# Performance work log

Measured on AMD Instinct MI355X. Metric: run time of the kernel, lower is better.

The kernel has to match this reference:

```python
import jax, jax.numpy as jnp
import numpy as np
from jax import lax

N_SKILLS = 10000
EMB = 128
HEADS = 4
DH = EMB // HEADS  # 32 per-head out channels
E_EDGES = 320000
B, T = 256, 200
RNN_H = 256
NEG_SLOPE = 0.2  # GATv2 LeakyReLU default


def setup_inputs() -> dict:
    key = jax.random.key(0)
    ks = jax.random.split(key, 32)
    inp = {}
    inp["skills_in"] = jax.random.randint(ks[0], (B, T), 0, N_SKILLS)
    inp["resp_in"] = jax.random.randint(ks[1], (B, T), 0, 2)
    lengths = jnp.sort(jax.random.randint(ks[2], (B,), 5, T + 1))[::-1]
    inp["lengths"] = lengths.at[0].set(T)  # enforce_sorted=True, max len = T
    inp["edge_index"] = jax.random.randint(ks[3], (2, E_EDGES), 0, N_SKILLS)
    inp["edge_weight"] = jax.random.uniform(ks[4], (E_EDGES,), dtype=jnp.float32)
    sc = 0.05
    inp["skill_emb_w"] = jax.random.normal(ks[5], (N_SKILLS, EMB), jnp.float32) * sc
    kidx = 6
    for l in range(2):
        inp[f"g{l}_Wl"] = jax.random.normal(ks[kidx + 0], (EMB, EMB), jnp.float32) * sc
        inp[f"g{l}_bl"] = jnp.zeros((EMB,), jnp.float32)
        inp[f"g{l}_Wr"] = jax.random.normal(ks[kidx + 1], (EMB, EMB), jnp.float32) * sc
        inp[f"g{l}_br"] = jnp.zeros((EMB,), jnp.float32)
        inp[f"g{l}_We"] = jax.random.normal(ks[kidx + 2], (EMB, 1), jnp.float32) * sc
        inp[f"g{l}_att"] = jax.random.normal(ks[kidx + 3], (HEADS, DH), jnp.float32) * sc
        inp[f"g{l}_bias"] = jnp.zeros((EMB,), jnp.float32)
        kidx += 4
    inp["resp_emb_w"] = jax.random.normal(ks[14], (2, EMB), jnp.float32) * sc
    inp["gru_Wih"] = jax.random.normal(ks[15], (3 * RNN_H, EMB), jnp.float32) * sc
    inp["gru_Whh"] = jax.random.normal(ks[16], (3 * RNN_H, RNN_H), jnp.float32) * sc
    inp["gru_bih"] = jnp.zeros((3 * RNN_H,), jnp.float32)
    inp["gru_bhh"] = jnp.zeros((3 * RNN_H,), jnp.float32)
    inp["proj_W"] = jax.random.normal(ks[17], (EMB, RNN_H), jnp.float32) * sc
    inp["proj_b"] = jnp.zeros((EMB,), jnp.float32)
    return inp


def _add_self_loops(edge_index, edge_weight):
    # PyG add_remaining_self_loops with fill_value='mean': loop attr = mean of
    # incoming edge attrs per target node (0 if no incoming edges).
    src, dst = edge_index[0], edge_index[1]
    ea = edge_weight.reshape(-1, 1)
    s = jax.ops.segment_sum(ea, dst, num_segments=N_SKILLS)
    c = jax.ops.segment_sum(jnp.ones_like(ea), dst, num_segments=N_SKILLS)
    loop_attr = s / jnp.maximum(c, 1.0)
    ar = jnp.arange(N_SKILLS, dtype=src.dtype)
    return (jnp.concatenate([src, ar]), jnp.concatenate([dst, ar]),
            jnp.concatenate([ea, loop_attr], axis=0))


def _gatv2_layer(h, src, dst, ea, Wl, bl, Wr, br, We, att, bias):
    xl = (h @ Wl.T + bl).reshape(-1, HEADS, DH)   # [N,H,D] lin_l
    xr = (h @ Wr.T + br).reshape(-1, HEADS, DH)   # [N,H,D] lin_r
    ee = (ea @ We.T).reshape(-1, HEADS, DH)       # [E,H,D] lin_edge (no bias)
    m = xl[src] + xr[dst] + ee                    # per-edge message pre-act
    m_act = jnp.where(m > 0, m, NEG_SLOPE * m)
    e = jnp.einsum('ehd,hd->eh', m_act, att)      # attention logits
    emax = jax.ops.segment_max(e, dst, num_segments=N_SKILLS)
    a = jnp.exp(e - emax[dst])
    denom = jax.ops.segment_sum(a, dst, num_segments=N_SKILLS)
    alpha = a / (denom[dst] + 1e-16)              # softmax over incoming edges
    out = jax.ops.segment_sum(alpha[:, :, None] * xl[src], dst,
                              num_segments=N_SKILLS)
    return out.reshape(-1, HEADS * DH) + bias


def _gru(x, lengths, Wih, Whh, bih, bhh):
    # Packed GRU emulation: state frozen and output zeroed past each length.
    Bb, Tt, _ = x.shape
    H = Whh.shape[1]
    xg = jnp.einsum('bte,ge->btg', x, Wih) + bih  # [B,T,3H], gates r|z|n
    mask = (jnp.arange(Tt)[None, :] < lengths[:, None])  # [B,T]

    def step(h, inp):
        xg_t, m_t = inp  # [B,3H], [B,1]
        hg = h @ Whh.T + bhh
        xr, xz, xn = jnp.split(xg_t, 3, axis=-1)
        hr, hz, hn = jnp.split(hg, 3, axis=-1)
        r = jax.nn.sigmoid(xr + hr)
        z = jax.nn.sigmoid(xz + hz)
        n = jnp.tanh(xn + r * hn)
        h_new = (1.0 - z) * n + z * h
        h_keep = jnp.where(m_t, h_new, h)
        y = jnp.where(m_t, h_new, 0.0)  # pad_packed_sequence zero-pads
        return h_keep, y

    h0 = jnp.zeros((Bb, H), x.dtype)
    _, ys = lax.scan(step, h0, (xg.transpose(1, 0, 2), mask.T[:, :, None]))
    return ys.transpose(1, 0, 2)  # [B,T,H]


def reference(skills_in, resp_in, lengths, edge_index, edge_weight,
              skill_emb_w,
              g0_Wl, g0_bl, g0_Wr, g0_br, g0_We, g0_att, g0_bias,
              g1_Wl, g1_bl, g1_Wr, g1_br, g1_We, g1_att, g1_bias,
              resp_emb_w, gru_Wih, gru_Whh, gru_bih, gru_bhh,
              proj_W, proj_b):
    src, dst, ea = _add_self_loops(edge_index, edge_weight)
    h = skill_emb_w
    h = jax.nn.elu(_gatv2_layer(h, src, dst, ea, g0_Wl, g0_bl, g0_Wr, g0_br,
                                g0_We, g0_att, g0_bias))
    h = jax.nn.elu(_gatv2_layer(h, src, dst, ea, g1_Wl, g1_bl, g1_Wr, g1_br,
                                g1_We, g1_att, g1_bias))
    skill_embs = h  # [N,EMB] (dropout is identity in eval)
    x = skill_embs[skills_in] + resp_emb_w[resp_in]  # [B,T,EMB]
    hseq = _gru(x, lengths, gru_Wih, gru_Whh, gru_bih, gru_bhh)
    h_proj = hseq @ proj_W.T + proj_b  # [B,T,EMB]
    return (h_proj, skill_embs)
```

## Files before the change

### kernel.cpp

```cpp
#include <hip/hip_runtime.h>

#define N_NODES 10000
#define EMB     128
#define NE      320000
#define NE_TOT  330000
#define NB      256
#define NTT     200
#define RH      256
#define G3      768

typedef unsigned short u16;
typedef u16    u16x8  __attribute__((ext_vector_type(8)));
typedef __bf16 bf16x8 __attribute__((ext_vector_type(8)));
typedef float  f32x4  __attribute__((ext_vector_type(4)));

static __device__ __forceinline__ float bf2f(u16 u){
  unsigned int x = ((unsigned int)u) << 16;
  return __builtin_bit_cast(float, x);
}
static __device__ __forceinline__ u16 f2bf(float f){
  unsigned int x = __builtin_bit_cast(unsigned int, f);
  x += 0x7fffu + ((x >> 16) & 1u);
  return (u16)(x >> 16);
}

static __device__ __forceinline__ void stage16(const u16* g, u16* lds_wavebase, u16* lds_lane){
#if __has_builtin(__builtin_amdgcn_global_load_lds)
  __builtin_amdgcn_global_load_lds(
      (const __attribute__((address_space(1))) unsigned int*)g,
      (__attribute__((address_space(3))) unsigned int*)lds_wavebase, 16, 0, 0);
  (void)lds_lane;
#else
  *(u16x8*)lds_lane = *(const u16x8*)g;
#endif
}

static __device__ __forceinline__ float self4(f32x4 v, int r){
  float lo = (r&1) ? v[1] : v[0];
  float hi = (r&1) ? v[3] : v[2];
  return (r&2) ? hi : lo;
}
static __device__ __forceinline__ f32x4 seltile(f32x4 a, f32x4 b, f32x4 c, f32x4 d, int jt){
  f32x4 r;
  #pragma unroll
  for(int e=0;e<4;++e){
    float ab = (jt&1) ? b[e] : a[e];
    float cd = (jt&1) ? d[e] : c[e];
    r[e] = (jt&2) ? cd : ab;
  }
  return r;
}

__global__ void k_deg(const int* __restrict__ eidx, const float* __restrict__ ew,
                      int* __restrict__ deg, float* __restrict__ wsum){
  int i = blockIdx.x*256 + threadIdx.x;
  if(i >= NE) return;
  int d = eidx[NE + i];
  atomicAdd(&deg[d], 1);
  atomicAdd(&wsum[d], ew[i]);
}

__global__ __launch_bounds__(1024) void k_scan(const int* __restrict__ deg,
                      float* __restrict__ wsum, int* __restrict__ off){
  __shared__ int part[1024];
  int tid = threadIdx.x;
  int n0 = tid*10;
  int s = 0;
  for(int i=0;i<10;++i){ int n=n0+i; if(n<N_NODES) s += deg[n]+1; }
  part[tid] = s;
  for(int i=0;i<10;++i){
    int n=n0+i;
    if(n<N_NODES){ int d=deg[n]; wsum[n] = wsum[n] / (float)(d>1?d:1); }
  }
  __syncthreads();
  for(int st=1; st<1024; st<<=1){
    int v = (tid>=st) ? part[tid-st] : 0;
    __syncthreads();
    part[tid] += v;
    __syncthreads();
  }
  int base = tid ? part[tid-1] : 0;
  for(int i=0;i<10;++i){ int n=n0+i; if(n<N_NODES){ off[n]=base; base += deg[n]+1; } }
  if(tid==999) off[N_NODES] = base;
}

__global__ void k_scatter(const int* __restrict__ eidx, const float* __restrict__ ew,
                          const float* __restrict__ la, const int* __restrict__ off,
                          int* __restrict__ fill, int* __restrict__ csrs, float* __restrict__ csrw){
  int i = blockIdx.x*256 + threadIdx.x;
  if(i >= NE_TOT) return;
  int s, d; float w;
  if(i < NE){ s = eidx[i]; d = eidx[NE+i]; w = ew[i]; }
  else      { int n = i-NE; s=n; d=n; w = la[n]; }
  int pos = off[d] + atomicAdd(&fill[d], 1);
  csrs[pos] = s; csrw[pos] = w;
}

#define WB_W   393216
#define WB_TOT (WB_W + N_NODES*EMB)
__global__ __launch_bounds__(256) void k_cvtall(
    const float* __restrict__ g0l, const float* __restrict__ g0r,
    const float* __restrict__ g1l, const float* __restrict__ g1r,
    const float* __restrict__ wih, const float* __restrict__ whh,
    const float* __restrict__ pw, const float* __restrict__ emb,
    u16* __restrict__ wb){
  int i = blockIdx.x*256 + threadIdx.x;
  if(i >= WB_TOT) return;
  float v;
  if(i < 65536){
    int seg = i >> 14, r = i & 16383;
    const float* s = (seg==0) ? g0l : (seg==1) ? g0r : (seg==2) ? g1l : g1r;
    v = s[r];
  } else if(i < 163840){ v = wih[i - 65536]; }
  else if(i < 360448){ v = whh[i - 163840]; }
  else if(i < WB_W)  { v = pw [i - 360448]; }
  else               { v = emb[i - WB_W]; }
  wb[i] = f2bf(v);
}

__global__ __launch_bounds__(256) void k_gather(
    const float* __restrict__ embN, const float* __restrict__ remb,
    const int* __restrict__ skills, const int* __restrict__ resp,
    u16* __restrict__ xemb){
  int i = blockIdx.x*256 + threadIdx.x;
  if(i >= NB*NTT*EMB/8) return;
  int row = i >> 4;
  int g8  = (i & 15) * 8;
  const float* ar = embN + (size_t)skills[row]*EMB + g8;
  const float* rr = remb + (size_t)resp[row]*EMB + g8;
  u16x8 v;
  #pragma unroll
  for(int e=0;e<8;++e) v[e] = f2bf(ar[e] + rr[e]);
  *(u16x8*)(xemb + (size_t)row*EMB + g8) = v;
}

template<int AMODE, bool OUTF32, int MI>
__global__ __launch_bounds__(256) void k_gemm(
    const u16* __restrict__ Av, const u16* __restrict__ W, const float* __restrict__ bias,
    void* __restrict__ out,
    int M, int N, int K,
    int t0, int chk,
    const int* __restrict__ lens)
{
  int tid = threadIdx.x;
  int wid = tid >> 6, l = tid & 63;
  int lr = l & 15, lg = l >> 4;
  int bm = blockIdx.x*(MI*64) + wid*(MI*16);
  int bn = blockIdx.y*64;
  f32x4 acc[MI][4] = {};
  int nk = K >> 5;
  for(int kt=0; kt<nk; ++kt){
    int k0 = kt*32 + lg*8;
    bf16x8 af[MI];
    #pragma unroll
    for(int mi=0; mi<MI; ++mi){
      int row = bm + mi*16 + lr;
      u16x8 v = {0,0,0,0,0,0,0,0};
      if(row < M){
        if constexpr(AMODE == 3){
          int b = row / chk, tt = row - b*chk;
          int arow = b*NTT + t0 + tt;
          v = *(const u16x8*)(Av + (size_t)arow*K + k0);
        } else {
          v = *(const u16x8*)(Av + (size_t)row*K + k0);
        }
      }
      af[mi] = __builtin_bit_cast(bf16x8, v);
    }
    #pragma unroll
    for(int nt=0; nt<4; ++nt){
      int col = bn + nt*16 + lr;
      u16x8 wv = *(const u16x8*)(W + (size_t)col*K + k0);
      bf16x8 bfr = __builtin_bit_cast(bf16x8, wv);
      #pragma unroll
      for(int mi=0; mi<MI; ++mi)
        acc[mi][nt] = __builtin_amdgcn_mfma_f32_16x16x32_bf16(af[mi], bfr, acc[mi][nt], 0,0,0);
    }
  }
  #pragma unroll
  for(int mi=0; mi<MI; ++mi){
    #pragma unroll
    for(int nt=0; nt<4; ++nt){
      int col = bn + nt*16 + lr;
      float bc = bias[col];
      #pragma unroll
      for(int r=0; r<4; ++r){
        int row = bm + mi*16 + lg*4 + r;
        if(row >= M) continue;
        float v = acc[mi][nt][r] + bc;
        if(lens){ int b = row/NTT; int t = row - b*NTT; if(t >= lens[b]) v = bc; }
        if constexpr(OUTF32) ((float*)out)[(size_t)row*N + col] = v;
        else                 ((u16*) out)[(size_t)row*N + col] = f2bf(v);
      }
    }
  }
}

template<bool BF16OUT>
__global__ __launch_bounds__(256) void k_attn(
    const int* __restrict__ off, const int* __restrict__ csrs, const float* __restrict__ csrw,
    const u16* __restrict__ xl, const u16* __restrict__ xr,
    const float* __restrict__ We, const float* __restrict__ att, const float* __restrict__ bias,
    float* __restrict__ houtF, u16* __restrict__ houtB)
{
  int wid = threadIdx.x >> 6, l = threadIdx.x & 63;
  int n = blockIdx.x*4 + wid;
  int d0 = 2*l;
  const unsigned int* xl2 = (const unsigned int*)xl;
  unsigned int xru = ((const unsigned int*)xr)[n*64 + l];
  float xrx = bf2f((u16)xru), xry = bf2f((u16)(xru>>16));
  float wex = We[d0],  wey = We[d0+1];
  float atx = att[d0], aty = att[d0+1];
  int p0 = off[n], p1 = off[n+1];
  float mx = -1e30f;
  for(int p=p0; p<p1; ++p){
    int s = csrs[p]; float w = csrw[p];
    unsigned int u = xl2[s*64 + l];
    float ax = bf2f((u16)u)       + xrx + w*wex;
    float ay = bf2f((u16)(u>>16)) + xry + w*wey;
    ax = ax > 0.f ? ax : 0.2f*ax;
    ay = ay > 0.f ? ay : 0.2f*ay;
    float c = ax*atx + ay*aty;
    c += __shfl_xor(c,1); c += __shfl_xor(c,2); c += __shfl_xor(c,4); c += __shfl_xor(c,8);
    mx = fmaxf(mx, c);
  }
  float den = 0.f, a0 = 0.f, a1 = 0.f;
  for(int p=p0; p<p1; ++p){
    int s = csrs[p]; float w = csrw[p];
    unsigned int u = xl2[s*64 + l];
    float xlx = bf2f((u16)u), xly = bf2f((u16)(u>>16));
    float ax = xlx + xrx + w*wex;
    float ay = xly + xry + w*wey;
    ax = ax > 0.f ? ax : 0.2f*ax;
    ay = ay > 0.f ? ay : 0.2f*ay;
    float c = ax*atx + ay*aty;
    c += __shfl_xor(c,1); c += __shfl_xor(c,2); c += __shfl_xor(c,4); c += __shfl_xor(c,8);
    float al = __expf(c - mx);
    den += al; a0 += al*xlx; a1 += al*xly;
  }
  float inv = 1.f/(den + 1e-16f);
  float o0 = a0*inv + bias[d0];
  float o1 = a1*inv + bias[d0+1];
  o0 = o0 > 0.f ? o0 : (__expf(o0) - 1.f);
  o1 = o1 > 0.f ? o1 : (__expf(o1) - 1.f);
  if constexpr(BF16OUT){
    houtB[n*EMB + d0]   = f2bf(o0);
    houtB[n*EMB + d0+1] = f2bf(o1);
  } else {
    houtF[n*EMB + d0]   = o0;
    houtF[n*EMB + d0+1] = o1;
  }
}


#define DECLW(nt) f32x4 wf_##nt##_0, wf_##nt##_1, wf_##nt##_2, wf_##nt##_3, \
                        wf_##nt##_4, wf_##nt##_5, wf_##nt##_6, wf_##nt##_7;

#define LDW1(nt,kt) { u16x8 wv = *(const u16x8*)(wr + (kt)*32 + lg*8); \
  wf_##nt##_##kt = __builtin_bit_cast(f32x4, wv); \
  asm volatile("" : "+a"(wf_##nt##_##kt)); }

#define LDW(nt) { int nrow = ((nt)>>2)*256 + wid*64 + ((nt)&3)*16 + lr; \
  const u16* wr = whb + (size_t)nrow*RH; \
  LDW1(nt,0) LDW1(nt,1) LDW1(nt,2) LDW1(nt,3) LDW1(nt,4) LDW1(nt,5) LDW1(nt,6) LDW1(nt,7) }

#define MFMA1(acc, wf, hf) asm volatile( \
  "v_mfma_f32_16x16x32_bf16 %0, %1, %2, %0" : "+v"(acc) : "a"(wf), "v"(hf));

#define MST(kt) { \
  f32x4 hf = __builtin_bit_cast(f32x4, *(const u16x8*)(hrd + (kt)*32 + lg*8)); \
  MFMA1(acc0,  wf_0_##kt,  hf) MFMA1(acc1,  wf_1_##kt,  hf) \
  MFMA1(acc2,  wf_2_##kt,  hf) MFMA1(acc3,  wf_3_##kt,  hf) \
  MFMA1(acc4,  wf_4_##kt,  hf) MFMA1(acc5,  wf_5_##kt,  hf) \
  MFMA1(acc6,  wf_6_##kt,  hf) MFMA1(acc7,  wf_7_##kt,  hf) \
  MFMA1(acc8,  wf_8_##kt,  hf) MFMA1(acc9,  wf_9_##kt,  hf) \
  MFMA1(acc10, wf_10_##kt, hf) MFMA1(acc11, wf_11_##kt, hf) }

__global__ __launch_bounds__(256,1) __attribute__((amdgpu_waves_per_eu(1,1))) void k_gru(
    const u16* __restrict__ xgc, const u16* __restrict__ whb, const float* __restrict__ bhh,
    const int* __restrict__ lens, u16* __restrict__ hseq, float* __restrict__ hsave,
    int t0, int t1, int chk)
{
  int tid = threadIdx.x;
  int wid = tid >> 6, l = tid & 63;
  int lr = l & 15, lg = l >> 4;
  int b = blockIdx.x;
  __shared__ __align__(16) u16 lds_h[2][256];
  __shared__ __align__(16) u16 lds_xg[2][1024];

  int mylen = lens[b];
  int tend = mylen < t1 ? mylen : t1;
  int nsteps = tend - t0; if(nsteps < 0) nsteps = 0;

  DECLW(0) DECLW(1) DECLW(2)  DECLW(3)  DECLW(4)  DECLW(5)
  DECLW(6) DECLW(7) DECLW(8)  DECLW(9)  DECLW(10) DECLW(11)
  LDW(0) LDW(1) LDW(2)  LDW(3)  LDW(4)  LDW(5)
  LDW(6) LDW(7) LDW(8)  LDW(9)  LDW(10) LDW(11)

  int jt   = lr >> 2;
  int rsel = lr & 3;
  int j    = wid*64 + jt*16 + lg*4 + rsel;
  float bhR = bhh[      j];
  float bhZ = bhh[256 + j];
  float bhN = bhh[512 + j];

  {
    u16 v = 0;
    if(t0 > 0) v = f2bf(hsave[(size_t)b*RH + tid]);
    lds_h[0][tid] = v;
  }
  float hst = (t0>0) ? hsave[(size_t)b*RH + j] : 0.f;

  int g = (wid==0) ? l : (64 + (l & 31));
  const u16* xsrc = xgc + ((size_t)b*chk)*G3 + g*8;
  int lwb = (wid==0) ? 0 : 512;

  if(nsteps > 0 && wid < 2)
    stage16(xsrc, &lds_xg[0][lwb], nullptr);
  xsrc += G3;
  asm volatile("s_waitcnt vmcnt(0)" ::: "memory");
  asm volatile("s_waitcnt lgkmcnt(0)" ::: "memory");
  __builtin_amdgcn_sched_barrier(0);
  __builtin_amdgcn_s_barrier();
  __builtin_amdgcn_sched_barrier(0);

  u16* outbase = hseq + ((size_t)b*NTT + t0)*RH;
  for(int s=0; s<nsteps; ++s){
    const u16* hrd = &lds_h[s&1][0];
    u16*       hwr = &lds_h[(s+1)&1][0];
    const u16* xgr = &lds_xg[s&1][0];
    int more = (s+1 < nsteps);

    if(more && wid < 2)
      stage16(xsrc, &lds_xg[(s+1)&1][lwb], nullptr);
    xsrc += G3;

    f32x4 acc0 = {}, acc1 = {}, acc2 = {}, acc3 = {}, acc4 = {}, acc5 = {},
          acc6 = {}, acc7 = {}, acc8 = {}, acc9 = {}, acc10 = {}, acc11 = {};
    MST(0) MST(1) MST(2) MST(3) MST(4) MST(5) MST(6) MST(7)

    {
      f32x4 aR = seltile(acc0, acc1, acc2,  acc3,  jt);
      f32x4 aZ = seltile(acc4, acc5, acc6,  acc7,  jt);
      f32x4 aN = seltile(acc8, acc9, acc10, acc11, jt);
      float hr = self4(aR, rsel) + bhR;
      float hz = self4(aZ, rsel) + bhZ;
      float hn = self4(aN, rsel) + bhN;
      float xrv = bf2f(xgr[      j]);
      float xzv = bf2f(xgr[256 + j]);
      float xnv = bf2f(xgr[512 + j]);
      float rg = 1.f/(1.f + __expf(-(xrv + hr)));
      float zg = 1.f/(1.f + __expf(-(xzv + hz)));
      float nn = xnv + rg*hn;
      float tg = 1.f - 2.f/(__expf(2.f*nn) + 1.f);
      float hv = (1.f - zg)*tg + zg*hst;
      hst = hv;
      u16 hb = f2bf(hv);
      hwr[j] = hb;
      outbase[j] = hb;
    }
    outbase += RH;

    if(more){
      asm volatile("s_waitcnt lgkmcnt(0)" ::: "memory");
      asm volatile("s_waitcnt vmcnt(1)" ::: "memory");
      __builtin_amdgcn_sched_barrier(0);
      __builtin_amdgcn_s_barrier();
      __builtin_amdgcn_sched_barrier(0);
    }
  }

  {
    u16* zp = outbase;
    for(int t = (tend > t0 ? tend : t0); t < t1; ++t){
      zp[j] = 0;
      zp += RH;
    }
  }

  hsave[(size_t)b*RH + j] = hst;
}

extern "C" void kernel_launch(void* const* d_in, const int* in_sizes, int n_in,
                              void* d_out, int out_size, void* d_ws, size_t ws_size,
                              hipStream_t stream){
  (void)in_sizes; (void)n_in; (void)out_size;
  const int*   skills = (const int*)d_in[0];
  const int*   resp   = (const int*)d_in[1];
  const int*   lens   = (const int*)d_in[2];
  const int*   eidx   = (const int*)d_in[3];
  const float* ew     = (const float*)d_in[4];
  const float* emb    = (const float*)d_in[5];
  const float* gW[2][7];
  for(int l2=0;l2<2;++l2) for(int j=0;j<7;++j) gW[l2][j] = (const float*)d_in[6 + l2*7 + j];
  const float* remb  = (const float*)d_in[20];
  const float* Wih   = (const float*)d_in[21];
  const float* Whh   = (const float*)d_in[22];
  const float* bih   = (const float*)d_in[23];
  const float* bhh   = (const float*)d_in[24];
  const float* projW = (const float*)d_in[25];
  const float* projb = (const float*)d_in[26];

  char* p = (char*)d_ws;
  size_t o = 0;
  auto take = [&](size_t bytes)->char*{ char* r = p + o; o = (o + bytes + 255) & ~(size_t)255; return r; };
  int*   deg  = (int*)  take(4*N_NODES);
  int*   fill = (int*)  take(4*N_NODES);
  float* wsum = (float*)take(4*N_NODES);
  size_t zbytes = o;
  int*   off   = (int*)  take(4*(N_NODES+1));
  int*   csrs  = (int*)  take(4*NE_TOT);
  float* csrw  = (float*)take(4*NE_TOT);
  u16*   xl    = (u16*)  take(2UL*N_NODES*EMB);
  u16*   xr    = (u16*)  take(2UL*N_NODES*EMB);
  u16*   h1b   = (u16*)  take(2UL*N_NODES*EMB);
  float* hsave = (float*)take(4UL*NB*RH);
  u16*   wb    = (u16*)  take(2UL*WB_TOT);
  u16*   hseq  = (u16*)  take(2UL*NB*NTT*RH);
  u16*   xemb  = (u16*)  take(2UL*NB*NTT*EMB);
  size_t fixed_end = o;
  int chk = 200;
  while(chk > 25 && fixed_end + 2UL*NB*(size_t)chk*G3 > ws_size) chk /= 2;
  u16*   xgc  = (u16*)  take(2UL*NB*(size_t)chk*G3);

  const u16* wb_g0l  = wb;
  const u16* wb_g0r  = wb + 16384;
  const u16* wb_g1l  = wb + 32768;
  const u16* wb_g1r  = wb + 49152;
  const u16* wb_wih  = wb + 65536;
  const u16* wb_whh  = wb + 163840;
  const u16* wb_proj = wb + 360448;
  const u16* wb_emb  = wb + WB_W;

  float* outP = (float*)d_out;
  float* outE = outP + (size_t)NB*NTT*EMB;

  hipMemsetAsync(d_ws, 0, zbytes, stream);
  k_deg<<<(NE+255)/256, 256, 0, stream>>>(eidx, ew, deg, wsum);
  k_scan<<<1, 1024, 0, stream>>>(deg, wsum, off);
  k_scatter<<<(NE_TOT+255)/256, 256, 0, stream>>>(eidx, ew, wsum, off, fill, csrs, csrw);
  k_cvtall<<<(WB_TOT+255)/256, 256, 0, stream>>>(gW[0][0], gW[0][2], gW[1][0], gW[1][2],
                                                 Wih, Whh, projW, emb, (u16*)wb);

  dim3 gN((N_NODES+127)/128, EMB/64);
  k_gemm<2,false,2><<<gN, 256, 0, stream>>>(wb_emb, wb_g0l, gW[0][1], xl, N_NODES, EMB, EMB,
                                 0, 0, nullptr);
  k_gemm<2,false,2><<<gN, 256, 0, stream>>>(wb_emb, wb_g0r, gW[0][3], xr, N_NODES, EMB, EMB,
                                 0, 0, nullptr);
  k_attn<true><<<N_NODES/4, 256, 0, stream>>>(off, csrs, csrw, xl, xr,
                                 gW[0][4], gW[0][5], gW[0][6], nullptr, h1b);
  k_gemm<2,false,2><<<gN, 256, 0, stream>>>(h1b, wb_g1l, gW[1][1], xl, N_NODES, EMB, EMB,
                                 0, 0, nullptr);
  k_gemm<2,false,2><<<gN, 256, 0, stream>>>(h1b, wb_g1r, gW[1][3], xr, N_NODES, EMB, EMB,
                                 0, 0, nullptr);
  k_attn<false><<<N_NODES/4, 256, 0, stream>>>(off, csrs, csrw, xl, xr,
                                 gW[1][4], gW[1][5], gW[1][6], outE, nullptr);

  k_gather<<<(NB*NTT*EMB/8 + 255)/256, 256, 0, stream>>>(outE, remb, skills, resp, xemb);

  for(int t0=0; t0<NTT; t0+=chk){
    k_gemm<3,false,4><<<dim3(NB*chk/256, G3/64), 256, 0, stream>>>(xemb, wb_wih, bih, xgc,
                                 NB*chk, G3, EMB, t0, chk, nullptr);
    k_gru<<<NB, 256, 0, stream>>>(xgc, wb_whh, bhh, lens, hseq, hsave, t0, t0+chk, chk);
  }
  k_gemm<2,true,4><<<dim3(NB*NTT/256, EMB/64), 256, 0, stream>>>(hseq, wb_proj, projb, outP,
                                 NB*NTT, EMB, RH, 0, 0, lens);
}
```

Baseline: 666.8 us.

## Merge prep kernels, batch left/right GAT GEMMs, triple-buffer GRU input staging

```diff
diff --git a/kernel.cpp b/kernel.cpp
--- a/kernel.cpp
+++ b/kernel.cpp
@@ -51,13 +51,40 @@
   return r;
 }
 
-__global__ void k_deg(const int* __restrict__ eidx, const float* __restrict__ ew,
-                      int* __restrict__ deg, float* __restrict__ wsum){
-  int i = blockIdx.x*256 + threadIdx.x;
-  if(i >= NE) return;
-  int d = eidx[NE + i];
-  atomicAdd(&deg[d], 1);
-  atomicAdd(&wsum[d], ew[i]);
+#define WB_W   393216
+#define WB_TOT (WB_W + N_NODES*EMB)
+#define NDEG_BLK ((NE + 255)/256)
+#define NCVT_BLK ((WB_TOT + 255)/256)
+__global__ __launch_bounds__(256) void k_prep(
+    const int* __restrict__ eidx, const float* __restrict__ ew,
+    int* __restrict__ deg, float* __restrict__ wsum,
+    const float* __restrict__ g0l, const float* __restrict__ g0r,
+    const float* __restrict__ g1l, const float* __restrict__ g1r,
+    const float* __restrict__ wih, const float* __restrict__ whh,
+    const float* __restrict__ pw, const float* __restrict__ emb,
+    u16* __restrict__ wb)
+{
+  int bid = blockIdx.x;
+  if(bid < NDEG_BLK){
+    int i = bid*256 + threadIdx.x;
+    if(i >= NE) return;
+    int d = eidx[NE + i];
+    atomicAdd(&deg[d], 1);
+    atomicAdd(&wsum[d], ew[i]);
+  } else {
+    int i = (bid - NDEG_BLK)*256 + threadIdx.x;
+    if(i >= WB_TOT) return;
+    float v;
+    if(i < 65536){
+      int seg = i >> 14, r = i & 16383;
+      const float* s = (seg==0) ? g0l : (seg==1) ? g0r : (seg==2) ? g1l : g1r;
+      v = s[r];
+    } else if(i < 163840){ v = wih[i - 65536]; }
+    else if(i < 360448){ v = whh[i - 163840]; }
+    else if(i < WB_W)  { v = pw [i - 360448]; }
+    else               { v = emb[i - WB_W]; }
+    wb[i] = f2bf(v);
+  }
 }
 
 __global__ __launch_bounds__(1024) void k_scan(const int* __restrict__ deg,
@@ -94,28 +121,6 @@
   else      { int n = i-NE; s=n; d=n; w = la[n]; }
   int pos = off[d] + atomicAdd(&fill[d], 1);
   csrs[pos] = s; csrw[pos] = w;
-}
-
-#define WB_W   393216
-#define WB_TOT (WB_W + N_NODES*EMB)
-__global__ __launch_bounds__(256) void k_cvtall(
-    const float* __restrict__ g0l, const float* __restrict__ g0r,
-    const float* __restrict__ g1l, const float* __restrict__ g1r,
-    const float* __restrict__ wih, const float* __restrict__ whh,
-    const float* __restrict__ pw, const float* __restrict__ emb,
-    u16* __restrict__ wb){
-  int i = blockIdx.x*256 + threadIdx.x;
-  if(i >= WB_TOT) return;
-  float v;
-  if(i < 65536){
-    int seg = i >> 14, r = i & 16383;
-    const float* s = (seg==0) ? g0l : (seg==1) ? g0r : (seg==2) ? g1l : g1r;
-    v = s[r];
-  } else if(i < 163840){ v = wih[i - 65536]; }
-  else if(i < 360448){ v = whh[i - 163840]; }
-  else if(i < WB_W)  { v = pw [i - 360448]; }
-  else               { v = emb[i - WB_W]; }
-  wb[i] = f2bf(v);
 }
 
 __global__ __launch_bounds__(256) void k_gather(
@@ -196,6 +201,58 @@
   }
 }
 
+__global__ __launch_bounds__(256) void k_gemm2(
+    const u16* __restrict__ Av,
+    const u16* __restrict__ W0, const u16* __restrict__ W1,
+    const float* __restrict__ b0, const float* __restrict__ b1,
+    u16* __restrict__ out0, u16* __restrict__ out1,
+    int M, int N, int K)
+{
+  const u16*   W    = blockIdx.z ? W1 : W0;
+  const float* bias = blockIdx.z ? b1 : b0;
+  u16*         out  = blockIdx.z ? out1 : out0;
+  int tid = threadIdx.x;
+  int wid = tid >> 6, l = tid & 63;
+  int lr = l & 15, lg = l >> 4;
+  int bm = blockIdx.x*128 + wid*32;
+  int bn = blockIdx.y*64;
+  f32x4 acc[2][4] = {};
+  int nk = K >> 5;
+  for(int kt=0; kt<nk; ++kt){
+    int k0 = kt*32 + lg*8;
+    bf16x8 af[2];
+    #pragma unroll
+    for(int mi=0; mi<2; ++mi){
+      int row = bm + mi*16 + lr;
+      u16x8 v = {0,0,0,0,0,0,0,0};
+      if(row < M) v = *(const u16x8*)(Av + (size_t)row*K + k0);
+      af[mi] = __builtin_bit_cast(bf16x8, v);
+    }
+    #pragma unroll
+    for(int nt=0; nt<4; ++nt){
+      int col = bn + nt*16 + lr;
+      u16x8 wv = *(const u16x8*)(W + (size_t)col*K + k0);
+      bf16x8 bfr = __builtin_bit_cast(bf16x8, wv);
+      acc[0][nt] = __builtin_amdgcn_mfma_f32_16x16x32_bf16(af[0], bfr, acc[0][nt], 0,0,0);
+      acc[1][nt] = __builtin_amdgcn_mfma_f32_16x16x32_bf16(af[1], bfr, acc[1][nt], 0,0,0);
+    }
+  }
+  #pragma unroll
+  for(int mi=0; mi<2; ++mi){
+    #pragma unroll
+    for(int nt=0; nt<4; ++nt){
+      int col = bn + nt*16 + lr;
+      float bc = bias[col];
+      #pragma unroll
+      for(int r=0; r<4; ++r){
+        int row = bm + mi*16 + lg*4 + r;
+        if(row >= M) continue;
+        out[(size_t)row*N + col] = f2bf(acc[mi][nt][r] + bc);
+      }
+    }
+  }
+}
+
 template<bool BF16OUT>
 __global__ __launch_bounds__(256) void k_attn(
     const int* __restrict__ off, const int* __restrict__ csrs, const float* __restrict__ csrw,
@@ -286,7 +343,7 @@
   int lr = l & 15, lg = l >> 4;
   int b = blockIdx.x;
   __shared__ __align__(16) u16 lds_h[2][256];
-  __shared__ __align__(16) u16 lds_xg[2][1024];
+  __shared__ __align__(16) u16 lds_xg[3][1024];
 
   int mylen = lens[b];
   int tend = mylen < t1 ? mylen : t1;
@@ -318,6 +375,9 @@
   if(nsteps > 0 && wid < 2)
     stage16(xsrc, &lds_xg[0][lwb], nullptr);
   xsrc += G3;
+  if(nsteps > 1 && wid < 2)
+    stage16(xsrc, &lds_xg[1][lwb], nullptr);
+  xsrc += G3;
   asm volatile("s_waitcnt vmcnt(0)" ::: "memory");
   asm volatile("s_waitcnt lgkmcnt(0)" ::: "memory");
   __builtin_amdgcn_sched_barrier(0);
@@ -328,11 +388,11 @@
   for(int s=0; s<nsteps; ++s){
     const u16* hrd = &lds_h[s&1][0];
     u16*       hwr = &lds_h[(s+1)&1][0];
-    const u16* xgr = &lds_xg[s&1][0];
+    const u16* xgr = &lds_xg[s%3][0];
     int more = (s+1 < nsteps);
 
-    if(more && wid < 2)
-      stage16(xsrc, &lds_xg[(s+1)&1][lwb], nullptr);
+    if(s+2 < nsteps && wid < 2)
+      stage16(xsrc, &lds_xg[(s+2)%3][lwb], nullptr);
     xsrc += G3;
 
     f32x4 acc0 = {}, acc1 = {}, acc2 = {}, acc3 = {}, acc4 = {}, acc5 = {},
@@ -363,7 +423,7 @@
 
     if(more){
       asm volatile("s_waitcnt lgkmcnt(0)" ::: "memory");
-      asm volatile("s_waitcnt vmcnt(1)" ::: "memory");
+      asm volatile("s_waitcnt vmcnt(3)" ::: "memory");
       __builtin_amdgcn_sched_barrier(0);
       __builtin_amdgcn_s_barrier();
       __builtin_amdgcn_sched_barrier(0);
@@ -436,23 +496,19 @@
   float* outE = outP + (size_t)NB*NTT*EMB;
 
   hipMemsetAsync(d_ws, 0, zbytes, stream);
-  k_deg<<<(NE+255)/256, 256, 0, stream>>>(eidx, ew, deg, wsum);
+  k_prep<<<NDEG_BLK + NCVT_BLK, 256, 0, stream>>>(eidx, ew, deg, wsum,
+                                 gW[0][0], gW[0][2], gW[1][0], gW[1][2],
+                                 Wih, Whh, projW, emb, (u16*)wb);
   k_scan<<<1, 1024, 0, stream>>>(deg, wsum, off);
   k_scatter<<<(NE_TOT+255)/256, 256, 0, stream>>>(eidx, ew, wsum, off, fill, csrs, csrw);
-  k_cvtall<<<(WB_TOT+255)/256, 256, 0, stream>>>(gW[0][0], gW[0][2], gW[1][0], gW[1][2],
-                                                 Wih, Whh, projW, emb, (u16*)wb);
-
-  dim3 gN((N_NODES+127)/128, EMB/64);
-  k_gemm<2,false,2><<<gN, 256, 0, stream>>>(wb_emb, wb_g0l, gW[0][1], xl, N_NODES, EMB, EMB,
-                                 0, 0, nullptr);
-  k_gemm<2,false,2><<<gN, 256, 0, stream>>>(wb_emb, wb_g0r, gW[0][3], xr, N_NODES, EMB, EMB,
-                                 0, 0, nullptr);
+
+  dim3 gN2((N_NODES+127)/128, EMB/64, 2);
+  k_gemm2<<<gN2, 256, 0, stream>>>(wb_emb, wb_g0l, wb_g0r, gW[0][1], gW[0][3],
+                                   xl, xr, N_NODES, EMB, EMB);
   k_attn<true><<<N_NODES/4, 256, 0, stream>>>(off, csrs, csrw, xl, xr,
                                  gW[0][4], gW[0][5], gW[0][6], nullptr, h1b);
-  k_gemm<2,false,2><<<gN, 256, 0, stream>>>(h1b, wb_g1l, gW[1][1], xl, N_NODES, EMB, EMB,
-                                 0, 0, nullptr);
-  k_gemm<2,false,2><<<gN, 256, 0, stream>>>(h1b, wb_g1r, gW[1][3], xr, N_NODES, EMB, EMB,
-                                 0, 0, nullptr);
+  k_gemm2<<<gN2, 256, 0, stream>>>(h1b, wb_g1l, wb_g1r, gW[1][1], gW[1][3],
+                                   xl, xr, N_NODES, EMB, EMB);
   k_attn<false><<<N_NODES/4, 256, 0, stream>>>(off, csrs, csrw, xl, xr,
                                  gW[1][4], gW[1][5], gW[1][6], outE, nullptr);
 
```

Result: no change. 656.3 us (-1.6%).
